# Optimization experiments

Measured on AMD Instinct MI355X. Metric: run time of the kernel, lower is better.

Reference implementation:

```python
import jax, jax.numpy as jnp
import numpy as np

NUM_GRAPHS = 128
EPS = 1e-5


def _instance_norm(x, seg, num_seg):
    # Per-graph instance norm over rows grouped by seg (PyG InstanceNorm, affine=False).
    ones = jnp.ones((x.shape[0], 1), x.dtype)
    cnt = jnp.maximum(jax.ops.segment_sum(ones, seg, num_segments=num_seg), 1.0)  # [G,1]
    mean = jax.ops.segment_sum(x, seg, num_segments=num_seg) / cnt               # [G,C]
    xc = x - mean[seg]
    var = jax.ops.segment_sum(xc * xc, seg, num_segments=num_seg) / cnt          # [G,C]
    return xc * jax.lax.rsqrt(var[seg] + EPS)


def setup_inputs() -> dict:
    key = jax.random.key(0)
    ks = jax.random.split(key, 8)
    N, E, H, G = 50000, 800000, 64, NUM_GRAPHS
    emb = jax.random.normal(ks[0], (N, H), dtype=jnp.float32)
    edge_index = jax.random.randint(ks[1], (2, E), 0, N, dtype=jnp.int64)
    batch = jnp.sort(jax.random.randint(ks[2], (N,), 0, G, dtype=jnp.int64))
    s1 = 1.0 / np.sqrt(2 * H)
    s2 = 1.0 / np.sqrt(4 * H)
    s3 = 1.0 / np.sqrt(H)
    return {
        "emb": emb,
        "edge_index": edge_index,
        "batch": batch,
        "W1": jax.random.normal(ks[3], (2 * H, 4 * H), dtype=jnp.float32) * s1,
        "b1": jnp.zeros((4 * H,), jnp.float32),
        "W2": jax.random.normal(ks[4], (4 * H, H), dtype=jnp.float32) * s2,
        "b2": jnp.zeros((H,), jnp.float32),
        "W3": jax.random.normal(ks[5], (H, 1), dtype=jnp.float32) * s3,
        "b3": jnp.zeros((1,), jnp.float32),
    }


def reference(emb, edge_index, batch, W1, b1, W2, b2, W3, b3):
    col, row = edge_index[0], edge_index[1]
    # Gather both endpoint embeddings and concat: [E, 2H]
    f12 = jnp.concatenate([emb[col], emb[row]], axis=-1)
    seg = batch[col]  # graph id per edge
    # MLP([2H, 4H, H, 1]): Linear -> InstanceNorm(batch) -> ReLU (dropout=identity in eval)
    h = jnp.maximum(_instance_norm(f12 @ W1 + b1, seg, NUM_GRAPHS), 0.0)
    h = jnp.maximum(_instance_norm(h @ W2 + b2, seg, NUM_GRAPHS), 0.0)
    att_log_logits = h @ W3 + b3  # [E, 1]
    return att_log_logits
```

## Files before the change

kernel.cpp:

```cpp
#include <hip/hip_runtime.h>
#include <hip/hip_bf16.h>
#include <stdint.h>

#define NG 128
#define EPSI 1e-5f

typedef __attribute__((ext_vector_type(8))) __bf16 bf16x8;
typedef __attribute__((ext_vector_type(4))) float f32x4;

union ABFrag { bf16x8 v; unsigned short u[8]; uint4 q; };
union U8 { uint4 q; unsigned short u[8]; };

__device__ __forceinline__ float b2f(unsigned short u){
  union { unsigned int i; float f; } v; v.i = ((unsigned int)u) << 16; return v.f;
}
__device__ __forceinline__ unsigned short f2b(float f){
  union { float f; unsigned int i; } v; v.f = f;
  unsigned int r = v.i + 0x7fffu + ((v.i >> 16) & 1u);
  return (unsigned short)(r >> 16);
}
__device__ __forceinline__ unsigned int pk2(float lo, float hi){
  unsigned int r;
  asm("v_cvt_pk_bf16_f32 %0, %1, %2" : "=v"(r) : "v"(lo), "v"(hi));
  return r;
}

__global__ void kprep(const float* __restrict__ emb, const float* __restrict__ W1,
                      const float* __restrict__ W2,
                      const int* __restrict__ ei, const int* __restrict__ batch,
                      unsigned short* __restrict__ embb, unsigned short* __restrict__ WcF,
                      unsigned short* __restrict__ W2F, unsigned int* __restrict__ hist,
                      unsigned int* __restrict__ nodeh, int N, int E){
  __shared__ unsigned int h[NG];
  for (int i = threadIdx.x; i < NG; i += 256) h[i] = 0;
  __syncthreads();
  int idx = blockIdx.x * 256 + threadIdx.x;
  int stride = gridDim.x * 256;
  int embCnt4 = N * 16;
  for (int i = idx; i < embCnt4; i += stride){
    float4 v = *(const float4*)(emb + (size_t)i * 4);
    ushort4 o; o.x = f2b(v.x); o.y = f2b(v.y); o.z = f2b(v.z); o.w = f2b(v.w);
    *(ushort4*)(embb + (size_t)i * 4) = o;
  }
  for (int i = idx; i < 32 * 2 * 64 * 8; i += stride){
    int j = i & 7, lane = (i >> 3) & 63, ks = (i >> 9) & 1, tn = i >> 10;
    int quad = lane >> 4, l15 = lane & 15;
    int k = ks * 32 + quad * 8 + j;
    int n = tn * 16 + l15;
    float wv = (n < 256) ? W1[k * 256 + n] : W1[(k + 64) * 256 + (n - 256)];
    WcF[i] = f2b(wv);
  }
  for (int i = idx; i < 4 * 8 * 64 * 8; i += stride){
    int j = i & 7, lane = (i >> 3) & 63, ks = (i >> 9) & 7, w = i >> 12;
    int quad = lane >> 4, l15 = lane & 15;
    W2F[i] = f2b(W2[(ks * 32 + quad * 8 + j) * 64 + w * 16 + l15]);
  }
  for (int e = idx; e < E; e += stride){
    int cn = ei[e];
    atomicAdd(&h[batch[cn]], 1u);
    atomicAdd(&nodeh[cn], 1u);
  }
  __syncthreads();
  for (int i = threadIdx.x; i < NG; i += 256)
    if (h[i]) atomicAdd(&hist[i], h[i]);
}

__global__ void __launch_bounds__(256) kscan(const unsigned int* __restrict__ nodeh,
                      const unsigned int* __restrict__ hist,
                      const int* __restrict__ batch,
                      unsigned int* __restrict__ ncursor,
                      unsigned int* __restrict__ gmeta, int N){
  __shared__ unsigned int sh[3];
  __shared__ unsigned int wtot[4];
  int g = blockIdx.x;
  int t = threadIdx.x;
  unsigned int part = 0;
  for (int i = t; i < g; i += 256) part += (hist[i] + 31u) & ~31u;
  #pragma unroll
  for (int d = 1; d < 64; d <<= 1) part += __shfl_xor(part, d);
  if ((t & 63) == 0) wtot[t >> 6] = part;
  if (t == 64 || t == 65){
    int target = g + (t - 64);
    int lo = 0, hi = N;
    while (lo < hi){ int mid = (lo + hi) >> 1; if (batch[mid] < target) lo = mid + 1; else hi = mid; }
    sh[1 + (t - 64)] = lo;
  }
  __syncthreads();
  if (t == 0){
    unsigned int pb = wtot[0] + wtot[1] + wtot[2] + wtot[3];
    sh[0] = pb;
    gmeta[g] = pb;
    if (g == NG - 1) gmeta[NG] = pb + ((hist[g] + 31u) & ~31u);
  }
  __syncthreads();
  unsigned int run = sh[0];
  int lo = (int)sh[1], hi = (int)sh[2];
  int wid = t >> 6;
  for (int base = lo; base < hi; base += 256){
    int i = base + t;
    unsigned int v = (i < hi) ? nodeh[i] : 0u;
    unsigned int x = v;
    #pragma unroll
    for (int d = 1; d < 64; d <<= 1){
      unsigned int y = __shfl_up(x, d);
      if ((t & 63) >= d) x += y;
    }
    if ((t & 63) == 63) wtot[wid] = x;
    __syncthreads();
    unsigned int woff = 0;
    #pragma unroll
    for (int wb = 0; wb < 4; ++wb) if (wb < wid) woff += wtot[wb];
    if (i < hi) ncursor[i] = run + woff + x - v;
    run += wtot[0] + wtot[1] + wtot[2] + wtot[3];
    __syncthreads();
  }
}

__global__ void kscatter(const int* __restrict__ ei, const int* __restrict__ batch, int E,
                         unsigned int* __restrict__ ncursor, int4* __restrict__ einfo){
  int idx = blockIdx.x * 256 + threadIdx.x;
  for (int e = idx; e < E; e += gridDim.x * 256){
    int cn = ei[e], rn = ei[E + e];
    int g = batch[cn];
    unsigned int p = atomicAdd(&ncursor[cn], 1u);
    einfo[p] = make_int4(cn, rn, g, e);
  }
}

__global__ void kpad(int4* __restrict__ einfo, const unsigned int* __restrict__ hist,
                     const unsigned int* __restrict__ gmeta){
  int g = blockIdx.x;
  unsigned int cnt = hist[g];
  if (!cnt) return;
  unsigned int pe = (cnt + 31u) & ~31u;
  if (cnt == pe) return;
  unsigned int base = gmeta[g];
  int4 e0 = einfo[base]; e0.w = -1;
  for (unsigned int i = cnt + threadIdx.x; i < pe; i += 64)
    einfo[base + i] = e0;
}

__global__ void __launch_bounds__(256) kgemm1(const unsigned short* __restrict__ embb,
    const unsigned short* __restrict__ WcF, const float* __restrict__ b1,
    unsigned short* __restrict__ PQb, int Nn){
  int wave = threadIdx.x >> 6, lane = threadIdx.x & 63;
  int quad = lane >> 4, l15 = lane & 15;
  int t = blockIdx.x * 4 + wave;
  int tmmax = (Nn + 15) >> 4;
  int tm = t >> 5, tn = t & 31;
  if (tm >= tmmax) return;
  int m = tm * 16 + l15; if (m >= Nn) m = Nn - 1;
  f32x4 acc = {0.f, 0.f, 0.f, 0.f};
  #pragma unroll
  for (int ks = 0; ks < 2; ++ks){
    ABFrag a, b;
    a.q = *(const uint4*)(embb + (size_t)m * 64 + ks * 32 + quad * 8);
    b.q = *(const uint4*)(WcF + ((size_t)(tn * 2 + ks) * 64 + lane) * 8);
    acc = __builtin_amdgcn_mfma_f32_16x16x32_bf16(a.v, b.v, acc, 0, 0, 0);
  }
  int col = tn * 16 + l15;
  float bias = (col < 256) ? b1[col] : 0.0f;
  #pragma unroll
  for (int r = 0; r < 4; ++r){
    int rowg = tm * 16 + quad * 4 + r;
    if (rowg < Nn) PQb[(size_t)rowg * 512 + col] = f2b(acc[r] + bias);
  }
}

__global__ void __launch_bounds__(256) kstats1(const unsigned short* __restrict__ PQb,
                        const int4* __restrict__ einfo, const unsigned int* __restrict__ gmeta,
                        float* __restrict__ sum1, float* __restrict__ sq1){
  __shared__ float lsum[8][256];
  __shared__ float lsq[8][256];
  int tid = threadIdx.x;
  int EP = (int)gmeta[NG];
  int i0 = blockIdx.x * 512;
  if (i0 >= EP) return;
  for (int i = tid; i < 8 * 256; i += 256){ ((float*)lsum)[i] = 0.f; ((float*)lsq)[i] = 0.f; }
  __syncthreads();
  int i1 = min(EP, i0 + 512);
  int gfirst = einfo[i0].z;
  int eo = tid >> 5;
  int c8 = (tid & 31) * 8;
  float s[8], q[8];
  #pragma unroll
  for (int t = 0; t < 8; ++t){ s[t] = 0.f; q[t] = 0.f; }
  int cur = -1;
  auto flushreg = [&](){
    if (cur >= 0){
      unsigned slot = (unsigned)(cur - gfirst);
      if (slot < 8u){
        #pragma unroll
        for (int t = 0; t < 8; ++t){
          atomicAdd(&lsum[slot][c8 + t], s[t]);
          atomicAdd(&lsq[slot][c8 + t], q[t]);
        }
      } else {
        #pragma unroll
        for (int t = 0; t < 8; ++t){
          atomicAdd(&sum1[cur * 256 + c8 + t], s[t]);
          atomicAdd(&sq1[cur * 256 + c8 + t], q[t]);
        }
      }
      #pragma unroll
      for (int t = 0; t < 8; ++t){ s[t] = 0.f; q[t] = 0.f; }
    }
  };
  for (int p = i0 + eo; p < i1; p += 16){
    int4 ev0 = einfo[p];
    int p2 = p + 8;
    int4 ev1 = (p2 < i1) ? einfo[p2] : make_int4(0, 0, -1, -1);
    U8 pu0, qu0, pu1, qu1;
    pu0.q = *(const uint4*)(PQb + (size_t)ev0.x * 512 + c8);
    qu0.q = *(const uint4*)(PQb + (size_t)ev0.y * 512 + 256 + c8);
    pu1.q = *(const uint4*)(PQb + (size_t)ev1.x * 512 + c8);
    qu1.q = *(const uint4*)(PQb + (size_t)ev1.y * 512 + 256 + c8);
    if (ev0.z != cur){ flushreg(); cur = ev0.z; }
    if (ev0.w >= 0){
      #pragma unroll
      for (int t = 0; t < 8; ++t){
        float y = b2f(pu0.u[t]) + b2f(qu0.u[t]);
        s[t] += y; q[t] += y * y;
      }
    }
    if (ev1.z >= 0){
      if (ev1.z != cur){ flushreg(); cur = ev1.z; }
      if (ev1.w >= 0){
        #pragma unroll
        for (int t = 0; t < 8; ++t){
          float y = b2f(pu1.u[t]) + b2f(qu1.u[t]);
          s[t] += y; q[t] += y * y;
        }
      }
    }
  }
  flushreg();
  __syncthreads();
  for (int i = tid; i < 8 * 256; i += 256){
    int slot = i >> 8, ch = i & 255;
    float vs = lsum[slot][ch], vq = lsq[slot][ch];
    if (vs != 0.f || vq != 0.f){
      int g = gfirst + slot;
      atomicAdd(&sum1[g * 256 + ch], vs);
      atomicAdd(&sq1[g * 256 + ch], vq);
    }
  }
}

__global__ void kfin(const float* __restrict__ sum, const float* __restrict__ sq,
                     const unsigned int* __restrict__ hist,
                     float* __restrict__ meanA, float* __restrict__ rstdA, int C){
  int i = blockIdx.x * blockDim.x + threadIdx.x;
  if (i >= NG * C) return;
  int g = i / C;
  float cnt = fmaxf((float)hist[g], 1.0f);
  float m = sum[i] / cnt;
  float v = sq[i] / cnt - m * m;
  meanA[i] = m;
  rstdA[i] = rsqrtf(fmaxf(v, 0.f) + EPSI);
}

__global__ void __launch_bounds__(256) knorm1(unsigned short* __restrict__ PQb,
    const int* __restrict__ batch, const float* __restrict__ mean1,
    const float* __restrict__ rstd1, int N){
  int idx = blockIdx.x * 256 + threadIdx.x;
  if (idx >= N * 32) return;
  int n = idx >> 5, c8 = (idx & 31) * 8;
  int g = batch[n];
  unsigned short* pp = PQb + (size_t)n * 512 + c8;
  U8 pu; pu.q = *(const uint4*)pp;
  const float* mg = mean1 + g * 256 + c8;
  const float* rg = rstd1 + g * 256 + c8;
  float4 m0 = *(const float4*)mg, m1 = *(const float4*)(mg + 4);
  float4 r0 = *(const float4*)rg, r1 = *(const float4*)(rg + 4);
  U8 o;
  o.q.x = pk2((b2f(pu.u[0]) - m0.x) * r0.x, (b2f(pu.u[1]) - m0.y) * r0.y);
  o.q.y = pk2((b2f(pu.u[2]) - m0.z) * r0.z, (b2f(pu.u[3]) - m0.w) * r0.w);
  o.q.z = pk2((b2f(pu.u[4]) - m1.x) * r1.x, (b2f(pu.u[5]) - m1.y) * r1.y);
  o.q.w = pk2((b2f(pu.u[6]) - m1.z) * r1.z, (b2f(pu.u[7]) - m1.w) * r1.w);
  *(uint4*)pp = o.q;
}

__global__ void __launch_bounds__(256, 5) kmain(const unsigned short* __restrict__ PQb,
    const unsigned short* __restrict__ W2F, const int4* __restrict__ einfo,
    const float* __restrict__ rstd1, const float* __restrict__ b2,
    const unsigned int* __restrict__ hist, const unsigned int* __restrict__ gmeta,
    unsigned short* __restrict__ y2b, float* __restrict__ sum2, float* __restrict__ sq2){
  __shared__ unsigned short Blds[4 * 8 * 64 * 8];
  {
    const uint4* src = (const uint4*)W2F;
    uint4* dst = (uint4*)Blds;
    for (int i = threadIdx.x; i < 2048; i += 256) dst[i] = src[i];
  }
  __syncthreads();
  int wave = threadIdx.x >> 6, lane = threadIdx.x & 63;
  int quad = lane >> 4, l15 = lane & 15;
  float b2v[4];
  #pragma unroll
  for (int cg = 0; cg < 4; ++cg) b2v[cg] = b2[cg * 16 + l15];
  int ntiles = (int)(gmeta[NG] >> 5);
  int nw = gridDim.x * 4;
  for (int t = blockIdx.x * 4 + wave; t < ntiles; t += nw){
    int p0 = t * 32;
    int4 ev0 = einfo[p0 + l15];
    int4 ev1 = einfo[p0 + 16 + l15];
    int g = __builtin_amdgcn_readfirstlane(ev0.z);
    const unsigned short* pp0 = PQb + (size_t)ev0.x * 512 + quad * 8;
    const unsigned short* qq0 = PQb + (size_t)ev0.y * 512 + 256 + quad * 8;
    const unsigned short* pp1 = PQb + (size_t)ev1.x * 512 + quad * 8;
    const unsigned short* qq1 = PQb + (size_t)ev1.y * 512 + 256 + quad * 8;
    const float* rr = rstd1 + g * 256 + quad * 8;
    f32x4 acc[8];
    #pragma unroll
    for (int i = 0; i < 8; ++i){ acc[i][0]=0.f; acc[i][1]=0.f; acc[i][2]=0.f; acc[i][3]=0.f; }
    #pragma unroll 2
    for (int ks = 0; ks < 8; ++ks){
      U8 pu0, qu0, pu1, qu1;
      pu0.q = *(const uint4*)(pp0 + ks * 32);
      qu0.q = *(const uint4*)(qq0 + ks * 32);
      pu1.q = *(const uint4*)(pp1 + ks * 32);
      qu1.q = *(const uint4*)(qq1 + ks * 32);
      float4 ra = *(const float4*)(rr + ks * 32);
      float4 rb = *(const float4*)(rr + ks * 32 + 4);
      ABFrag a0, a1;
      a0.q.x = pk2(fmaxf(0.f, b2f(pu0.u[0]) + b2f(qu0.u[0]) * ra.x),
                   fmaxf(0.f, b2f(pu0.u[1]) + b2f(qu0.u[1]) * ra.y));
      a0.q.y = pk2(fmaxf(0.f, b2f(pu0.u[2]) + b2f(qu0.u[2]) * ra.z),
                   fmaxf(0.f, b2f(pu0.u[3]) + b2f(qu0.u[3]) * ra.w));
      a0.q.z = pk2(fmaxf(0.f, b2f(pu0.u[4]) + b2f(qu0.u[4]) * rb.x),
                   fmaxf(0.f, b2f(pu0.u[5]) + b2f(qu0.u[5]) * rb.y));
      a0.q.w = pk2(fmaxf(0.f, b2f(pu0.u[6]) + b2f(qu0.u[6]) * rb.z),
                   fmaxf(0.f, b2f(pu0.u[7]) + b2f(qu0.u[7]) * rb.w));
      a1.q.x = pk2(fmaxf(0.f, b2f(pu1.u[0]) + b2f(qu1.u[0]) * ra.x),
                   fmaxf(0.f, b2f(pu1.u[1]) + b2f(qu1.u[1]) * ra.y));
      a1.q.y = pk2(fmaxf(0.f, b2f(pu1.u[2]) + b2f(qu1.u[2]) * ra.z),
                   fmaxf(0.f, b2f(pu1.u[3]) + b2f(qu1.u[3]) * ra.w));
      a1.q.z = pk2(fmaxf(0.f, b2f(pu1.u[4]) + b2f(qu1.u[4]) * rb.x),
                   fmaxf(0.f, b2f(pu1.u[5]) + b2f(qu1.u[5]) * rb.y));
      a1.q.w = pk2(fmaxf(0.f, b2f(pu1.u[6]) + b2f(qu1.u[6]) * rb.z),
                   fmaxf(0.f, b2f(pu1.u[7]) + b2f(qu1.u[7]) * rb.w));
      #pragma unroll
      for (int cg = 0; cg < 4; ++cg){
        ABFrag b;
        b.q = *(const uint4*)&Blds[((cg * 8 + ks) * 64 + lane) * 8];
        acc[cg]     = __builtin_amdgcn_mfma_f32_16x16x32_bf16(a0.v, b.v, acc[cg], 0, 0, 0);
        acc[4 + cg] = __builtin_amdgcn_mfma_f32_16x16x32_bf16(a1.v, b.v, acc[4 + cg], 0, 0, 0);
      }
    }
    int nl = (int)gmeta[g] + (int)hist[g] - p0;
    #pragma unroll
    for (int cg = 0; cg < 4; ++cg){
      float s = 0.f, qs = 0.f;
      #pragma unroll
      for (int sub = 0; sub < 2; ++sub)
        #pragma unroll
        for (int r = 0; r < 4; ++r){
          float y = acc[sub * 4 + cg][r] + b2v[cg];
          int el = sub * 16 + quad * 4 + r;
          y2b[(size_t)(p0 + el) * 64 + cg * 16 + l15] = f2b(y);
          if (el < nl){ s += y; qs = fmaf(y, y, qs); }
        }
      s  += __shfl_xor(s, 16);  s  += __shfl_xor(s, 32);
      qs += __shfl_xor(qs, 16); qs += __shfl_xor(qs, 32);
      if (quad == 0){
        atomicAdd(&sum2[g * 64 + cg * 16 + l15], s);
        atomicAdd(&sq2[g * 64 + cg * 16 + l15], qs);
      }
    }
  }
}

__global__ void kfinal(const unsigned short* __restrict__ y2b, const int4* __restrict__ einfo,
                       const unsigned int* __restrict__ gmeta,
                       const float* __restrict__ mean2, const float* __restrict__ rstd2,
                       const float* __restrict__ W3, const float* __restrict__ b3,
                       float* __restrict__ out){
  int EP = (int)gmeta[NG];
  int sub = threadIdx.x & 7;
  int c8 = sub * 8;
  float w3r[8];
  #pragma unroll
  for (int t = 0; t < 8; ++t) w3r[t] = W3[c8 + t];
  float b3v = b3[0];
  int step = (gridDim.x * blockDim.x) >> 3;
  for (int i = (blockIdx.x * blockDim.x + threadIdx.x) >> 3; i < EP; i += step){
    int4 ev = einfo[i];
    U8 yv; yv.q = *(const uint4*)(y2b + (size_t)i * 64 + c8);
    const float* mg = mean2 + ev.z * 64 + c8;
    const float* rg = rstd2 + ev.z * 64 + c8;
    float4 m0 = *(const float4*)mg, m1 = *(const float4*)(mg + 4);
    float4 r0 = *(const float4*)rg, r1 = *(const float4*)(rg + 4);
    float a = 0.f;
    a += fmaxf(0.f, (b2f(yv.u[0]) - m0.x) * r0.x) * w3r[0];
    a += fmaxf(0.f, (b2f(yv.u[1]) - m0.y) * r0.y) * w3r[1];
    a += fmaxf(0.f, (b2f(yv.u[2]) - m0.z) * r0.z) * w3r[2];
    a += fmaxf(0.f, (b2f(yv.u[3]) - m0.w) * r0.w) * w3r[3];
    a += fmaxf(0.f, (b2f(yv.u[4]) - m1.x) * r1.x) * w3r[4];
    a += fmaxf(0.f, (b2f(yv.u[5]) - m1.y) * r1.y) * w3r[5];
    a += fmaxf(0.f, (b2f(yv.u[6]) - m1.z) * r1.z) * w3r[6];
    a += fmaxf(0.f, (b2f(yv.u[7]) - m1.w) * r1.w) * w3r[7];
    a += __shfl_xor(a, 1);
    a += __shfl_xor(a, 2);
    a += __shfl_xor(a, 4);
    if (sub == 0 && ev.w >= 0) out[ev.w] = a + b3v;
  }
}

extern "C" void kernel_launch(void* const* d_in, const int* in_sizes, int n_in,
                              void* d_out, int out_size, void* d_ws, size_t ws_size,
                              hipStream_t stream){
  const float* emb  = (const float*)d_in[0];
  const int*   ei   = (const int*)d_in[1];
  const int*   batch= (const int*)d_in[2];
  const float* W1   = (const float*)d_in[3];
  const float* b1   = (const float*)d_in[4];
  const float* W2   = (const float*)d_in[5];
  const float* b2   = (const float*)d_in[6];
  const float* W3   = (const float*)d_in[7];
  const float* b3   = (const float*)d_in[8];
  int N = in_sizes[0] / 64;
  int E = in_sizes[1] / 2;
  int EPMAX = E + NG * 32;
  float* out = (float*)d_out;

  char* w = (char*)d_ws;
  size_t off = 0;
  auto nxt = [&](size_t bytes) -> char* {
    char* p = w + off;
    off = (off + bytes + 255) & ~(size_t)255;
    return p;
  };
  unsigned short* embb = (unsigned short*)nxt((size_t)N * 64 * 2);
  unsigned short* WcF  = (unsigned short*)nxt(32 * 2 * 64 * 8 * 2);
  unsigned short* W2F  = (unsigned short*)nxt(4 * 8 * 64 * 8 * 2);
  unsigned short* PQb  = (unsigned short*)nxt((size_t)N * 512 * 2);
  unsigned short* y2b  = (unsigned short*)nxt((size_t)EPMAX * 64 * 2);
  int4* einfo = (int4*)nxt((size_t)EPMAX * 16);
  float* mean1 = (float*)nxt(NG * 256 * 4);
  float* rstd1 = (float*)nxt(NG * 256 * 4);
  float* mean2 = (float*)nxt(NG * 64 * 4);
  float* rstd2 = (float*)nxt(NG * 64 * 4);
  unsigned int* ncursor = (unsigned int*)nxt((size_t)N * 4);
  unsigned int* gmeta   = (unsigned int*)nxt((NG + 1) * 4);
  char* zbase = w + off;
  unsigned int* hist  = (unsigned int*)nxt(NG * 4);
  unsigned int* nodeh = (unsigned int*)nxt((size_t)N * 4);
  float* sum1 = (float*)nxt(NG * 256 * 4);
  float* sq1  = (float*)nxt(NG * 256 * 4);
  float* sum2 = (float*)nxt(NG * 64 * 4);
  float* sq2  = (float*)nxt(NG * 64 * 4);
  size_t zbytes = (size_t)((w + off) - zbase);
  hipMemsetAsync(zbase, 0, zbytes, stream);

  kprep<<<2048, 256, 0, stream>>>(emb, W1, W2, ei, batch, embb, WcF, W2F, hist, nodeh, N, E);
  kscan<<<NG, 256, 0, stream>>>(nodeh, hist, batch, ncursor, gmeta, N);
  kscatter<<<2048, 256, 0, stream>>>(ei, batch, E, ncursor, einfo);
  kpad<<<NG, 64, 0, stream>>>(einfo, hist, gmeta);
  {
    int tiles = ((N + 15) / 16) * 32;
    kgemm1<<<(tiles + 3) / 4, 256, 0, stream>>>(embb, WcF, b1, PQb, N);
  }
  kstats1<<<(EPMAX + 511) / 512, 256, 0, stream>>>(PQb, einfo, gmeta, sum1, sq1);
  kfin<<<(NG * 256 + 255) / 256, 256, 0, stream>>>(sum1, sq1, hist, mean1, rstd1, 256);
  knorm1<<<(N * 32 + 255) / 256, 256, 0, stream>>>(PQb, batch, mean1, rstd1, N);
  kmain<<<2048, 256, 0, stream>>>(PQb, W2F, einfo, rstd1, b2, hist, gmeta, y2b, sum2, sq2);
  kfin<<<(NG * 64 + 255) / 256, 256, 0, stream>>>(sum2, sq2, hist, mean2, rstd2, 64);
  kfinal<<<2048, 256, 0, stream>>>(y2b, einfo, gmeta, mean2, rstd2, W3, b3, out);
}
```

Measured before the change: 512.9 us.

## Fold first instance-norm into main GEMM and prefetch edge operands

Removes the separate knorm1 pass over the node projection buffer. kfin now also emits mean*rstd, so kmain applies normalization as fma(P+Q, rstd, -mean*rstd) before the ReLU, which is algebraically the same as the old result. kmain also gets a three-deep register prefetch ring for the gathered P/Q rows, fully unrolls its k loop and relaxes launch bounds from 5 to 4 waves. kstats1 processes four edges per iteration instead of two to keep more gathers in flight. In exchange there is more register pressure and lower occupancy in kmain, plus small bf16 rounding differences.

```diff
diff --git a/kernel.cpp b/kernel.cpp
--- a/kernel.cpp
+++ b/kernel.cpp
@@ -206,32 +206,41 @@
       for (int t = 0; t < 8; ++t){ s[t] = 0.f; q[t] = 0.f; }
     }
   };
-  for (int p = i0 + eo; p < i1; p += 16){
+  auto accum = [&](const U8& pu, const U8& qu){
+    #pragma unroll
+    for (int t = 0; t < 8; ++t){
+      float y = b2f(pu.u[t]) + b2f(qu.u[t]);
+      s[t] += y; q[t] += y * y;
+    }
+  };
+  for (int p = i0 + eo; p < i1; p += 32){
     int4 ev0 = einfo[p];
-    int p2 = p + 8;
-    int4 ev1 = (p2 < i1) ? einfo[p2] : make_int4(0, 0, -1, -1);
-    U8 pu0, qu0, pu1, qu1;
+    int pa = p + 8, pb = p + 16, pc = p + 24;
+    int4 ev1 = (pa < i1) ? einfo[pa] : make_int4(0, 0, -1, -1);
+    int4 ev2 = (pb < i1) ? einfo[pb] : make_int4(0, 0, -1, -1);
+    int4 ev3 = (pc < i1) ? einfo[pc] : make_int4(0, 0, -1, -1);
+    U8 pu0, qu0, pu1, qu1, pu2, qu2, pu3, qu3;
     pu0.q = *(const uint4*)(PQb + (size_t)ev0.x * 512 + c8);
     qu0.q = *(const uint4*)(PQb + (size_t)ev0.y * 512 + 256 + c8);
     pu1.q = *(const uint4*)(PQb + (size_t)ev1.x * 512 + c8);
     qu1.q = *(const uint4*)(PQb + (size_t)ev1.y * 512 + 256 + c8);
+    pu2.q = *(const uint4*)(PQb + (size_t)ev2.x * 512 + c8);
+    qu2.q = *(const uint4*)(PQb + (size_t)ev2.y * 512 + 256 + c8);
+    pu3.q = *(const uint4*)(PQb + (size_t)ev3.x * 512 + c8);
+    qu3.q = *(const uint4*)(PQb + (size_t)ev3.y * 512 + 256 + c8);
     if (ev0.z != cur){ flushreg(); cur = ev0.z; }
-    if (ev0.w >= 0){
-      #pragma unroll
-      for (int t = 0; t < 8; ++t){
-        float y = b2f(pu0.u[t]) + b2f(qu0.u[t]);
-        s[t] += y; q[t] += y * y;
-      }
-    }
+    if (ev0.w >= 0) accum(pu0, qu0);
     if (ev1.z >= 0){
       if (ev1.z != cur){ flushreg(); cur = ev1.z; }
-      if (ev1.w >= 0){
-        #pragma unroll
-        for (int t = 0; t < 8; ++t){
-          float y = b2f(pu1.u[t]) + b2f(qu1.u[t]);
-          s[t] += y; q[t] += y * y;
-        }
-      }
+      if (ev1.w >= 0) accum(pu1, qu1);
+    }
+    if (ev2.z >= 0){
+      if (ev2.z != cur){ flushreg(); cur = ev2.z; }
+      if (ev2.w >= 0) accum(pu2, qu2);
+    }
+    if (ev3.z >= 0){
+      if (ev3.z != cur){ flushreg(); cur = ev3.z; }
+      if (ev3.w >= 0) accum(pu3, qu3);
     }
   }
   flushreg();
@@ -249,41 +258,24 @@
 
 __global__ void kfin(const float* __restrict__ sum, const float* __restrict__ sq,
                      const unsigned int* __restrict__ hist,
-                     float* __restrict__ meanA, float* __restrict__ rstdA, int C){
+                     float* __restrict__ meanA, float* __restrict__ rstdA,
+                     float* __restrict__ mrA, int C){
   int i = blockIdx.x * blockDim.x + threadIdx.x;
   if (i >= NG * C) return;
   int g = i / C;
   float cnt = fmaxf((float)hist[g], 1.0f);
   float m = sum[i] / cnt;
   float v = sq[i] / cnt - m * m;
+  float r = rsqrtf(fmaxf(v, 0.f) + EPSI);
   meanA[i] = m;
-  rstdA[i] = rsqrtf(fmaxf(v, 0.f) + EPSI);
-}
-
-__global__ void __launch_bounds__(256) knorm1(unsigned short* __restrict__ PQb,
-    const int* __restrict__ batch, const float* __restrict__ mean1,
-    const float* __restrict__ rstd1, int N){
-  int idx = blockIdx.x * 256 + threadIdx.x;
-  if (idx >= N * 32) return;
-  int n = idx >> 5, c8 = (idx & 31) * 8;
-  int g = batch[n];
-  unsigned short* pp = PQb + (size_t)n * 512 + c8;
-  U8 pu; pu.q = *(const uint4*)pp;
-  const float* mg = mean1 + g * 256 + c8;
-  const float* rg = rstd1 + g * 256 + c8;
-  float4 m0 = *(const float4*)mg, m1 = *(const float4*)(mg + 4);
-  float4 r0 = *(const float4*)rg, r1 = *(const float4*)(rg + 4);
-  U8 o;
-  o.q.x = pk2((b2f(pu.u[0]) - m0.x) * r0.x, (b2f(pu.u[1]) - m0.y) * r0.y);
-  o.q.y = pk2((b2f(pu.u[2]) - m0.z) * r0.z, (b2f(pu.u[3]) - m0.w) * r0.w);
-  o.q.z = pk2((b2f(pu.u[4]) - m1.x) * r1.x, (b2f(pu.u[5]) - m1.y) * r1.y);
-  o.q.w = pk2((b2f(pu.u[6]) - m1.z) * r1.z, (b2f(pu.u[7]) - m1.w) * r1.w);
-  *(uint4*)pp = o.q;
-}
-
-__global__ void __launch_bounds__(256, 5) kmain(const unsigned short* __restrict__ PQb,
+  rstdA[i] = r;
+  mrA[i] = m * r;
+}
+
+__global__ void __launch_bounds__(256, 4) kmain(const unsigned short* __restrict__ PQb,
     const unsigned short* __restrict__ W2F, const int4* __restrict__ einfo,
-    const float* __restrict__ rstd1, const float* __restrict__ b2,
+    const float* __restrict__ mr1, const float* __restrict__ rstd1,
+    const float* __restrict__ b2,
     const unsigned int* __restrict__ hist, const unsigned int* __restrict__ gmeta,
     unsigned short* __restrict__ y2b, float* __restrict__ sum2, float* __restrict__ sq2){
   __shared__ unsigned short Blds[4 * 8 * 64 * 8];
@@ -310,35 +302,48 @@
     const unsigned short* pp1 = PQb + (size_t)ev1.x * 512 + quad * 8;
     const unsigned short* qq1 = PQb + (size_t)ev1.y * 512 + 256 + quad * 8;
     const float* rr = rstd1 + g * 256 + quad * 8;
+    const float* mm = mr1   + g * 256 + quad * 8;
     f32x4 acc[8];
     #pragma unroll
     for (int i = 0; i < 8; ++i){ acc[i][0]=0.f; acc[i][1]=0.f; acc[i][2]=0.f; acc[i][3]=0.f; }
-    #pragma unroll 2
+    U8 bp0[3], bq0[3], bp1[3], bq1[3];
+    #pragma unroll
+    for (int d = 0; d < 3; ++d){
+      bp0[d].q = *(const uint4*)(pp0 + d * 32);
+      bq0[d].q = *(const uint4*)(qq0 + d * 32);
+      bp1[d].q = *(const uint4*)(pp1 + d * 32);
+      bq1[d].q = *(const uint4*)(qq1 + d * 32);
+    }
+    #pragma unroll
     for (int ks = 0; ks < 8; ++ks){
-      U8 pu0, qu0, pu1, qu1;
-      pu0.q = *(const uint4*)(pp0 + ks * 32);
-      qu0.q = *(const uint4*)(qq0 + ks * 32);
-      pu1.q = *(const uint4*)(pp1 + ks * 32);
-      qu1.q = *(const uint4*)(qq1 + ks * 32);
+      const int sl = ks % 3;
       float4 ra = *(const float4*)(rr + ks * 32);
       float4 rb = *(const float4*)(rr + ks * 32 + 4);
+      float4 ma = *(const float4*)(mm + ks * 32);
+      float4 mb = *(const float4*)(mm + ks * 32 + 4);
       ABFrag a0, a1;
-      a0.q.x = pk2(fmaxf(0.f, b2f(pu0.u[0]) + b2f(qu0.u[0]) * ra.x),
-                   fmaxf(0.f, b2f(pu0.u[1]) + b2f(qu0.u[1]) * ra.y));
-      a0.q.y = pk2(fmaxf(0.f, b2f(pu0.u[2]) + b2f(qu0.u[2]) * ra.z),
-                   fmaxf(0.f, b2f(pu0.u[3]) + b2f(qu0.u[3]) * ra.w));
-      a0.q.z = pk2(fmaxf(0.f, b2f(pu0.u[4]) + b2f(qu0.u[4]) * rb.x),
-                   fmaxf(0.f, b2f(pu0.u[5]) + b2f(qu0.u[5]) * rb.y));
-      a0.q.w = pk2(fmaxf(0.f, b2f(pu0.u[6]) + b2f(qu0.u[6]) * rb.z),
-                   fmaxf(0.f, b2f(pu0.u[7]) + b2f(qu0.u[7]) * rb.w));
-      a1.q.x = pk2(fmaxf(0.f, b2f(pu1.u[0]) + b2f(qu1.u[0]) * ra.x),
-                   fmaxf(0.f, b2f(pu1.u[1]) + b2f(qu1.u[1]) * ra.y));
-      a1.q.y = pk2(fmaxf(0.f, b2f(pu1.u[2]) + b2f(qu1.u[2]) * ra.z),
-                   fmaxf(0.f, b2f(pu1.u[3]) + b2f(qu1.u[3]) * ra.w));
-      a1.q.z = pk2(fmaxf(0.f, b2f(pu1.u[4]) + b2f(qu1.u[4]) * rb.x),
-                   fmaxf(0.f, b2f(pu1.u[5]) + b2f(qu1.u[5]) * rb.y));
-      a1.q.w = pk2(fmaxf(0.f, b2f(pu1.u[6]) + b2f(qu1.u[6]) * rb.z),
-                   fmaxf(0.f, b2f(pu1.u[7]) + b2f(qu1.u[7]) * rb.w));
+      a0.q.x = pk2(fmaxf(0.f, fmaf(b2f(bp0[sl].u[0]) + b2f(bq0[sl].u[0]), ra.x, -ma.x)),
+                   fmaxf(0.f, fmaf(b2f(bp0[sl].u[1]) + b2f(bq0[sl].u[1]), ra.y, -ma.y)));
+      a0.q.y = pk2(fmaxf(0.f, fmaf(b2f(bp0[sl].u[2]) + b2f(bq0[sl].u[2]), ra.z, -ma.z)),
+                   fmaxf(0.f, fmaf(b2f(bp0[sl].u[3]) + b2f(bq0[sl].u[3]), ra.w, -ma.w)));
+      a0.q.z = pk2(fmaxf(0.f, fmaf(b2f(bp0[sl].u[4]) + b2f(bq0[sl].u[4]), rb.x, -mb.x)),
+                   fmaxf(0.f, fmaf(b2f(bp0[sl].u[5]) + b2f(bq0[sl].u[5]), rb.y, -mb.y)));
+      a0.q.w = pk2(fmaxf(0.f, fmaf(b2f(bp0[sl].u[6]) + b2f(bq0[sl].u[6]), rb.z, -mb.z)),
+                   fmaxf(0.f, fmaf(b2f(bp0[sl].u[7]) + b2f(bq0[sl].u[7]), rb.w, -mb.w)));
+      a1.q.x = pk2(fmaxf(0.f, fmaf(b2f(bp1[sl].u[0]) + b2f(bq1[sl].u[0]), ra.x, -ma.x)),
+                   fmaxf(0.f, fmaf(b2f(bp1[sl].u[1]) + b2f(bq1[sl].u[1]), ra.y, -ma.y)));
+      a1.q.y = pk2(fmaxf(0.f, fmaf(b2f(bp1[sl].u[2]) + b2f(bq1[sl].u[2]), ra.z, -ma.z)),
+                   fmaxf(0.f, fmaf(b2f(bp1[sl].u[3]) + b2f(bq1[sl].u[3]), ra.w, -ma.w)));
+      a1.q.z = pk2(fmaxf(0.f, fmaf(b2f(bp1[sl].u[4]) + b2f(bq1[sl].u[4]), rb.x, -mb.x)),
+                   fmaxf(0.f, fmaf(b2f(bp1[sl].u[5]) + b2f(bq1[sl].u[5]), rb.y, -mb.y)));
+      a1.q.w = pk2(fmaxf(0.f, fmaf(b2f(bp1[sl].u[6]) + b2f(bq1[sl].u[6]), rb.z, -mb.z)),
+                   fmaxf(0.f, fmaf(b2f(bp1[sl].u[7]) + b2f(bq1[sl].u[7]), rb.w, -mb.w)));
+      if (ks < 5){
+        bp0[sl].q = *(const uint4*)(pp0 + (ks + 3) * 32);
+        bq0[sl].q = *(const uint4*)(qq0 + (ks + 3) * 32);
+        bp1[sl].q = *(const uint4*)(pp1 + (ks + 3) * 32);
+        bq1[sl].q = *(const uint4*)(qq1 + (ks + 3) * 32);
+      }
       #pragma unroll
       for (int cg = 0; cg < 4; ++cg){
         ABFrag b;
@@ -438,8 +443,10 @@
   int4* einfo = (int4*)nxt((size_t)EPMAX * 16);
   float* mean1 = (float*)nxt(NG * 256 * 4);
   float* rstd1 = (float*)nxt(NG * 256 * 4);
+  float* mr1   = (float*)nxt(NG * 256 * 4);
   float* mean2 = (float*)nxt(NG * 64 * 4);
   float* rstd2 = (float*)nxt(NG * 64 * 4);
+  float* mr2   = (float*)nxt(NG * 64 * 4);
   unsigned int* ncursor = (unsigned int*)nxt((size_t)N * 4);
   unsigned int* gmeta   = (unsigned int*)nxt((NG + 1) * 4);
   char* zbase = w + off;
@@ -461,9 +468,8 @@
     kgemm1<<<(tiles + 3) / 4, 256, 0, stream>>>(embb, WcF, b1, PQb, N);
   }
   kstats1<<<(EPMAX + 511) / 512, 256, 0, stream>>>(PQb, einfo, gmeta, sum1, sq1);
-  kfin<<<(NG * 256 + 255) / 256, 256, 0, stream>>>(sum1, sq1, hist, mean1, rstd1, 256);
-  knorm1<<<(N * 32 + 255) / 256, 256, 0, stream>>>(PQb, batch, mean1, rstd1, N);
-  kmain<<<2048, 256, 0, stream>>>(PQb, W2F, einfo, rstd1, b2, hist, gmeta, y2b, sum2, sq2);
-  kfin<<<(NG * 64 + 255) / 256, 256, 0, stream>>>(sum2, sq2, hist, mean2, rstd2, 64);
+  kfin<<<(NG * 256 + 255) / 256, 256, 0, stream>>>(sum1, sq1, hist, mean1, rstd1, mr1, 256);
+  kmain<<<2048, 256, 0, stream>>>(PQb, W2F, einfo, mr1, rstd1, b2, hist, gmeta, y2b, sum2, sq2);
+  kfin<<<(NG * 64 + 255) / 256, 256, 0, stream>>>(sum2, sq2, hist, mean2, rstd2, mr2, 64);
   kfinal<<<2048, 256, 0, stream>>>(y2b, einfo, gmeta, mean2, rstd2, W3, b3, out);
 }
```

Result: no change. 518.9 us (+1.2%).

## Use atomic tile counter in kmain and deepen gather unroll in kstats1

Applied to the files above, without the earlier changes.

kmain switches from a static grid-stride tile assignment to dynamic work stealing through a global atomic counter, prefetching the next tile index. The grid shrinks to 1280 blocks, matching the 5-blocks-per-CU launch bound. kstats1 unrolls its edge loop to four gathered edges per iteration for more memory-level parallelism. The cost is one atomic per tile plus higher register pressure in kstats1.

```diff
diff --git a/kernel.cpp b/kernel.cpp
--- a/kernel.cpp
+++ b/kernel.cpp
@@ -206,32 +206,41 @@
       for (int t = 0; t < 8; ++t){ s[t] = 0.f; q[t] = 0.f; }
     }
   };
-  for (int p = i0 + eo; p < i1; p += 16){
+  auto accum = [&](const U8& pu, const U8& qu){
+    #pragma unroll
+    for (int t = 0; t < 8; ++t){
+      float y = b2f(pu.u[t]) + b2f(qu.u[t]);
+      s[t] += y; q[t] += y * y;
+    }
+  };
+  for (int p = i0 + eo; p < i1; p += 32){
     int4 ev0 = einfo[p];
-    int p2 = p + 8;
-    int4 ev1 = (p2 < i1) ? einfo[p2] : make_int4(0, 0, -1, -1);
-    U8 pu0, qu0, pu1, qu1;
+    int pa = p + 8, pb = p + 16, pc = p + 24;
+    int4 ev1 = (pa < i1) ? einfo[pa] : make_int4(0, 0, -1, -1);
+    int4 ev2 = (pb < i1) ? einfo[pb] : make_int4(0, 0, -1, -1);
+    int4 ev3 = (pc < i1) ? einfo[pc] : make_int4(0, 0, -1, -1);
+    U8 pu0, qu0, pu1, qu1, pu2, qu2, pu3, qu3;
     pu0.q = *(const uint4*)(PQb + (size_t)ev0.x * 512 + c8);
     qu0.q = *(const uint4*)(PQb + (size_t)ev0.y * 512 + 256 + c8);
     pu1.q = *(const uint4*)(PQb + (size_t)ev1.x * 512 + c8);
     qu1.q = *(const uint4*)(PQb + (size_t)ev1.y * 512 + 256 + c8);
+    pu2.q = *(const uint4*)(PQb + (size_t)ev2.x * 512 + c8);
+    qu2.q = *(const uint4*)(PQb + (size_t)ev2.y * 512 + 256 + c8);
+    pu3.q = *(const uint4*)(PQb + (size_t)ev3.x * 512 + c8);
+    qu3.q = *(const uint4*)(PQb + (size_t)ev3.y * 512 + 256 + c8);
     if (ev0.z != cur){ flushreg(); cur = ev0.z; }
-    if (ev0.w >= 0){
-      #pragma unroll
-      for (int t = 0; t < 8; ++t){
-        float y = b2f(pu0.u[t]) + b2f(qu0.u[t]);
-        s[t] += y; q[t] += y * y;
-      }
-    }
+    if (ev0.w >= 0) accum(pu0, qu0);
     if (ev1.z >= 0){
       if (ev1.z != cur){ flushreg(); cur = ev1.z; }
-      if (ev1.w >= 0){
-        #pragma unroll
-        for (int t = 0; t < 8; ++t){
-          float y = b2f(pu1.u[t]) + b2f(qu1.u[t]);
-          s[t] += y; q[t] += y * y;
-        }
-      }
+      if (ev1.w >= 0) accum(pu1, qu1);
+    }
+    if (ev2.z >= 0){
+      if (ev2.z != cur){ flushreg(); cur = ev2.z; }
+      if (ev2.w >= 0) accum(pu2, qu2);
+    }
+    if (ev3.z >= 0){
+      if (ev3.z != cur){ flushreg(); cur = ev3.z; }
+      if (ev3.w >= 0) accum(pu3, qu3);
     }
   }
   flushreg();
@@ -285,6 +294,7 @@
     const unsigned short* __restrict__ W2F, const int4* __restrict__ einfo,
     const float* __restrict__ rstd1, const float* __restrict__ b2,
     const unsigned int* __restrict__ hist, const unsigned int* __restrict__ gmeta,
+    unsigned int* __restrict__ tilectr,
     unsigned short* __restrict__ y2b, float* __restrict__ sum2, float* __restrict__ sq2){
   __shared__ unsigned short Blds[4 * 8 * 64 * 8];
   {
@@ -293,14 +303,19 @@
     for (int i = threadIdx.x; i < 2048; i += 256) dst[i] = src[i];
   }
   __syncthreads();
-  int wave = threadIdx.x >> 6, lane = threadIdx.x & 63;
+  int lane = threadIdx.x & 63;
   int quad = lane >> 4, l15 = lane & 15;
   float b2v[4];
   #pragma unroll
   for (int cg = 0; cg < 4; ++cg) b2v[cg] = b2[cg * 16 + l15];
   int ntiles = (int)(gmeta[NG] >> 5);
-  int nw = gridDim.x * 4;
-  for (int t = blockIdx.x * 4 + wave; t < ntiles; t += nw){
+  int t;
+  if (lane == 0) t = (int)atomicAdd(tilectr, 1u);
+  t = __builtin_amdgcn_readfirstlane(t);
+  while (t < ntiles){
+    int tn;
+    if (lane == 0) tn = (int)atomicAdd(tilectr, 1u);
+    tn = __builtin_amdgcn_readfirstlane(tn);
     int p0 = t * 32;
     int4 ev0 = einfo[p0 + l15];
     int4 ev1 = einfo[p0 + 16 + l15];
@@ -367,6 +382,7 @@
         atomicAdd(&sq2[g * 64 + cg * 16 + l15], qs);
       }
     }
+    t = tn;
   }
 }
 
@@ -445,6 +461,7 @@
   char* zbase = w + off;
   unsigned int* hist  = (unsigned int*)nxt(NG * 4);
   unsigned int* nodeh = (unsigned int*)nxt((size_t)N * 4);
+  unsigned int* tilectr = (unsigned int*)nxt(256);
   float* sum1 = (float*)nxt(NG * 256 * 4);
   float* sq1  = (float*)nxt(NG * 256 * 4);
   float* sum2 = (float*)nxt(NG * 64 * 4);
@@ -463,7 +480,8 @@
   kstats1<<<(EPMAX + 511) / 512, 256, 0, stream>>>(PQb, einfo, gmeta, sum1, sq1);
   kfin<<<(NG * 256 + 255) / 256, 256, 0, stream>>>(sum1, sq1, hist, mean1, rstd1, 256);
   knorm1<<<(N * 32 + 255) / 256, 256, 0, stream>>>(PQb, batch, mean1, rstd1, N);
-  kmain<<<2048, 256, 0, stream>>>(PQb, W2F, einfo, rstd1, b2, hist, gmeta, y2b, sum2, sq2);
+  kmain<<<1280, 256, 0, stream>>>(PQb, W2F, einfo, rstd1, b2, hist, gmeta, tilectr,
+                                  y2b, sum2, sq2);
   kfin<<<(NG * 64 + 255) / 256, 256, 0, stream>>>(sum2, sq2, hist, mean2, rstd2, 64);
   kfinal<<<2048, 256, 0, stream>>>(y2b, einfo, gmeta, mean2, rstd2, W3, b3, out);
 }
```

New measurement: 780.0 us. +52.1%, slower.
